# Performance work log

Measured on AMD Instinct MI355X. Metric: run time of the kernel, lower is better.

The kernel has to match this reference:

```python
import jax, jax.numpy as jnp
import numpy as np

B, S, D, H = 256, 100, 512, 8
HD = D // H  # head_dim = 64


def setup_inputs() -> dict:
    key = jax.random.key(0)
    ks = jax.random.split(key, 12)
    scale = 1.0 / np.sqrt(D)
    return {
        "x": jax.random.normal(ks[0], (B, S, D), dtype=jnp.float32),
        "pos_emb": jax.random.normal(ks[1], (1, 100, D), dtype=jnp.float32),
        "temporal_decay": jnp.float32(0.95),
        # torch nn.Linear weights are [out, in]; applied as x @ W.T + b
        "Wq": jax.random.normal(ks[2], (D, D), dtype=jnp.float32) * scale,
        "bq": jax.random.normal(ks[3], (D,), dtype=jnp.float32) * scale,
        "Wk": jax.random.normal(ks[4], (D, D), dtype=jnp.float32) * scale,
        "bk": jax.random.normal(ks[5], (D,), dtype=jnp.float32) * scale,
        "Wv": jax.random.normal(ks[6], (D, D), dtype=jnp.float32) * scale,
        "bv": jax.random.normal(ks[7], (D,), dtype=jnp.float32) * scale,
        "Wo": jax.random.normal(ks[8], (D, D), dtype=jnp.float32) * scale,
        "bo": jax.random.normal(ks[9], (D,), dtype=jnp.float32) * scale,
    }


def reference(x, pos_emb, temporal_decay, Wq, bq, Wk, bk, Wv, bv, Wo, bo):
    b, s, d = x.shape
    xp = x + pos_emb[:, :s, :]  # add position embeddings to Q/K input only

    def heads(t):  # [b,s,d] -> [b,H,s,HD]
        return t.reshape(b, s, H, HD).transpose(0, 2, 1, 3)

    q = heads(xp @ Wq.T + bq)
    k = heads(xp @ Wk.T + bk)
    v = heads(x @ Wv.T + bv)  # V uses x WITHOUT positions (per source)

    scores = jnp.einsum("bhqd,bhkd->bhqk", q, k) / np.sqrt(HD)
    # decay over KEY positions: decay^(s-1), ..., decay^1, decay^0
    exponents = jnp.arange(s - 1, -1, -1, dtype=jnp.float32)
    decay = temporal_decay ** exponents  # [s]
    scores = scores * decay[None, None, None, :]

    attn = jax.nn.softmax(scores, axis=-1)  # dropout is identity in eval
    ctx = jnp.einsum("bhqk,bhkd->bhqd", attn, v)
    ctx = ctx.transpose(0, 2, 1, 3).reshape(b, s, d)
    out = ctx @ Wo.T + bo
    return out, attn
```

## Files before the change

kernel.cpp:

```cpp
#include <hip/hip_runtime.h>
#include <hip/hip_bf16.h>
#include <cmath>

#define B_   256
#define S_   100
#define D_   512
#define H_   8
#define HD_  64
#define BS_  (B_ * S_)
#define OUT_ELEMS  (BS_ * D_)
#define ATTN_ELEMS (B_ * H_ * S_ * S_)
#define DD_  (D_ * D_)

typedef __bf16 bf16x8 __attribute__((ext_vector_type(8)));
typedef float  f32x4  __attribute__((ext_vector_type(4)));

__device__ __forceinline__ void gload16(const void* g, void* l) {
    __builtin_amdgcn_global_load_lds(
        (const __attribute__((address_space(1))) void*)g,
        (__attribute__((address_space(3))) void*)l, 16, 0, 0);
}

__device__ __forceinline__ void stage_tile(const __hip_bfloat16* __restrict__ src,
                                           char* ldsTile, int t) {
    #pragma unroll
    for (int i = 0; i < 4; ++i) {
        const int ci  = i * 256 + t;
        const int row = ci >> 3;
        const int sc  = (ci & 7) ^ (row & 7);
        gload16(src + (size_t)row * D_ + sc * 8,
                ldsTile + ((i * 256 + (t & 192)) << 4));
    }
}

__device__ __forceinline__ void stage_tile_h(const __hip_bfloat16* __restrict__ src,
                                             char* ldsTile, int t) {
    #pragma unroll
    for (int i = 0; i < 2; ++i) {
        const int ci  = i * 256 + t;
        const int row = ci >> 3;
        const int sc  = (ci & 7) ^ (row & 7);
        gload16(src + (size_t)row * D_ + sc * 8,
                ldsTile + ((i * 256 + (t & 192)) << 4));
    }
}

__device__ __forceinline__ void compute_fused(const char* buf, int lane,
                                              int wr, int wc,
                                              f32x4 acc[3][4][2]) {
    const int frow = lane & 15;
    const int fk   = lane >> 4;
    #pragma unroll
    for (int kk = 0; kk < 2; ++kk) {
        const int ch = kk * 4 + fk;
        bf16x8 af[4];
        #pragma unroll
        for (int m = 0; m < 4; ++m) {
            const int row = wr + m * 16 + frow;
            af[m] = *(const bf16x8*)(buf + row * 128 + ((ch ^ (row & 7)) << 4));
        }
        bf16x8 bfr[3][2];
        #pragma unroll
        for (int z = 0; z < 3; ++z)
            #pragma unroll
            for (int n = 0; n < 2; ++n) {
                const int row = wc + n * 16 + frow;
                bfr[z][n] = *(const bf16x8*)(buf + 16384 + z * 8192
                                             + row * 128 + ((ch ^ (row & 7)) << 4));
            }
        __builtin_amdgcn_s_setprio(1);
        #pragma unroll
        for (int z = 0; z < 3; ++z)
            #pragma unroll
            for (int m = 0; m < 4; ++m)
                #pragma unroll
                for (int n = 0; n < 2; ++n)
                    acc[z][m][n] = __builtin_amdgcn_mfma_f32_16x16x32_bf16(
                        af[m], bfr[z][n], acc[z][m][n], 0, 0, 0);
        __builtin_amdgcn_s_setprio(0);
    }
}

__device__ __forceinline__ void compute_tile_h(const char* ldsA, const char* ldsB,
                                               int lane, int wr, int wc,
                                               f32x4 acc[4][2]) {
    const int frow = lane & 15;
    const int fk   = lane >> 4;
    #pragma unroll
    for (int kk = 0; kk < 2; ++kk) {
        const int ch = kk * 4 + fk;
        bf16x8 af[4], bfr[2];
        #pragma unroll
        for (int m = 0; m < 4; ++m) {
            const int row = wr + m * 16 + frow;
            af[m] = *(const bf16x8*)(ldsA + row * 128 + ((ch ^ (row & 7)) << 4));
        }
        #pragma unroll
        for (int n = 0; n < 2; ++n) {
            const int row = wc + n * 16 + frow;
            bfr[n] = *(const bf16x8*)(ldsB + row * 128 + ((ch ^ (row & 7)) << 4));
        }
        __builtin_amdgcn_s_setprio(1);
        #pragma unroll
        for (int m = 0; m < 4; ++m)
            #pragma unroll
            for (int n = 0; n < 2; ++n)
                acc[m][n] = __builtin_amdgcn_mfma_f32_16x16x32_bf16(
                    af[m], bfr[n], acc[m][n], 0, 0, 0);
        __builtin_amdgcn_s_setprio(0);
    }
}

__global__ __launch_bounds__(256) void qkv_gemm(
    const __hip_bfloat16* __restrict__ apos,
    const __hip_bfloat16* __restrict__ wall,
    const float* __restrict__ bq, const float* __restrict__ bk,
    const float* __restrict__ bv, const float* __restrict__ pv,
    __hip_bfloat16* __restrict__ qkv)
{
    __shared__ __align__(16) char lds[2][40960];
    const int t    = threadIdx.x;
    const int r0   = blockIdx.x * 128, c0 = blockIdx.y * 64;
    const int lane = t & 63, wid = t >> 6;
    const int wr   = (wid >> 1) << 6;
    const int wc   = (wid & 1) << 5;

    f32x4 acc[3][4][2] = {};

    const __hip_bfloat16* Ab = apos + (size_t)r0 * D_;

    stage_tile(Ab, lds[0], t);
    #pragma unroll
    for (int z = 0; z < 3; ++z)
        stage_tile_h(wall + (size_t)z * DD_ + (size_t)c0 * D_,
                     lds[0] + 16384 + z * 8192, t);
    asm volatile("s_waitcnt vmcnt(0)" ::: "memory");
    __syncthreads();

    int cur = 0;
    for (int kt = 1; kt < 8; ++kt) {
        stage_tile(Ab + kt * 64, lds[cur ^ 1], t);
        #pragma unroll
        for (int z = 0; z < 3; ++z)
            stage_tile_h(wall + (size_t)z * DD_ + (size_t)c0 * D_ + kt * 64,
                         lds[cur ^ 1] + 16384 + z * 8192, t);
        compute_fused(lds[cur], lane, wr, wc, acc);
        asm volatile("s_waitcnt vmcnt(0)" ::: "memory");
        __syncthreads();
        cur ^= 1;
    }
    compute_fused(lds[cur], lane, wr, wc, acc);

    const int fcol = lane & 15, fq = lane >> 4;
    #pragma unroll
    for (int z = 0; z < 3; ++z) {
        const float* bias = (z == 0) ? bq : (z == 1) ? bk : bv;
        __hip_bfloat16* outz = qkv + (size_t)z * OUT_ELEMS;
        #pragma unroll
        for (int n = 0; n < 2; ++n) {
            const int c  = c0 + wc + n * 16 + fcol;
            const float bi = bias[c];
            const int h = c >> 6, hd = c & 63;
            #pragma unroll
            for (int m = 0; m < 4; ++m) {
                const int rbase = r0 + wr + m * 16 + fq * 4;
                #pragma unroll
                for (int r = 0; r < 4; ++r) {
                    const int rowg = rbase + r;
                    const int b = rowg / S_;
                    const int s = rowg - b * S_;
                    float v = acc[z][m][n][r] + bi;
                    if (z == 2) v -= pv[s * D_ + c];
                    outz[(((size_t)b * H_ + h) * S_ + s) * HD_ + hd] =
                        __float2bfloat16(v);
                }
            }
        }
    }
}

__global__ __launch_bounds__(256) void outproj_gemm(
    const __hip_bfloat16* __restrict__ ctx,
    const __hip_bfloat16* __restrict__ Wo,
    const float* __restrict__ bo,
    float* __restrict__ out)
{
    __shared__ __align__(16) char lds[2][24576];
    const int t    = threadIdx.x;
    const int r0   = blockIdx.x * 128, c0 = blockIdx.y * 64;
    const int lane = t & 63, wid = t >> 6;
    const int wr   = (wid >> 1) << 6, wc = (wid & 1) << 5;

    f32x4 acc[4][2] = {};

    const __hip_bfloat16* Ab = ctx + (size_t)r0 * D_;
    const __hip_bfloat16* Bb = Wo  + (size_t)c0 * D_;

    stage_tile(Ab, lds[0], t);
    stage_tile_h(Bb, lds[0] + 16384, t);
    asm volatile("s_waitcnt vmcnt(0)" ::: "memory");
    __syncthreads();

    int cur = 0;
    for (int kt = 1; kt < 8; ++kt) {
        stage_tile(Ab + kt * 64, lds[cur ^ 1], t);
        stage_tile_h(Bb + kt * 64, lds[cur ^ 1] + 16384, t);
        compute_tile_h(lds[cur], lds[cur] + 16384, lane, wr, wc, acc);
        asm volatile("s_waitcnt vmcnt(0)" ::: "memory");
        __syncthreads();
        cur ^= 1;
    }
    compute_tile_h(lds[cur], lds[cur] + 16384, lane, wr, wc, acc);

    const int fcol = lane & 15, fq = lane >> 4;
    #pragma unroll
    for (int n = 0; n < 2; ++n) {
        const int c  = c0 + wc + n * 16 + fcol;
        const float bi = bo[c];
        #pragma unroll
        for (int m = 0; m < 4; ++m) {
            const int rbase = r0 + wr + m * 16 + fq * 4;
            #pragma unroll
            for (int r = 0; r < 4; ++r) {
                const int rowg = rbase + r;
                out[(size_t)rowg * D_ + c] = acc[m][n][r] + bi;
            }
        }
    }
}

__global__ __launch_bounds__(256) void attn_mfma(
    const __hip_bfloat16* __restrict__ qkv,
    float* __restrict__ attn_out,
    __hip_bfloat16* __restrict__ ctx,
    const float* __restrict__ td_ptr)
{
    __shared__ __align__(16) __hip_bfloat16 Vt[2][64][136];
    __shared__ __align__(16) __hip_bfloat16 Pl[4][16][136];
    __shared__ float dec[128];

    const int t    = threadIdx.x;
    const int lane = t & 63, wid = t >> 6;
    const int c    = lane & 15, g4 = lane >> 4;
    const int bh0  = blockIdx.x * 2;

    if (t < 128)
        dec[t] = (t < S_) ? 0.125f * powf(td_ptr[0], (float)(S_ - 1 - t)) : 0.f;

    {
        const int h = wid >> 1;
        const int k = ((wid & 1) << 6) + lane;
        if (k < S_) {
            const __hip_bfloat16* vr = qkv + 2 * (size_t)OUT_ELEMS
                                     + (size_t)(bh0 + h) * (S_ * HD_)
                                     + (size_t)k * HD_;
            #pragma unroll
            for (int j8 = 0; j8 < 8; ++j8) {
                uint4 u = *(const uint4*)(vr + j8 * 8);
                const __hip_bfloat16* e = (const __hip_bfloat16*)&u;
                #pragma unroll
                for (int ee = 0; ee < 8; ++ee)
                    Vt[h][j8 * 8 + ee][k] = e[ee];
            }
        }
        for (int idx = t; idx < 2 * 64 * 9; idx += 256) {
            const int hh  = idx / 576;
            const int rem = idx - hh * 576;
            const int d   = rem / 9, c8 = rem - d * 9;
            *(double*)((char*)&Vt[hh][d][100] + c8 * 8) = 0.0;
        }
    }
    *(double*)&Pl[wid][c][112 + 4 * g4] = 0.0;
    __syncthreads();

    float decr[7][4];
    #pragma unroll
    for (int kt = 0; kt < 7; ++kt)
        #pragma unroll
        for (int r = 0; r < 4; ++r)
            decr[kt][r] = dec[16 * kt + 4 * g4 + r];

    for (int item = wid; item < 14; item += 4) {
        const int hh = item / 7;
        const int qt = item - hh * 7;
        const int bh = bh0 + hh;
        const __hip_bfloat16* Qb = qkv + (size_t)bh * (S_ * HD_);
        const __hip_bfloat16* Kb = qkv + (size_t)OUT_ELEMS + (size_t)bh * (S_ * HD_);

        const bf16x8 qf0 = *(const bf16x8*)(Qb + (16 * qt + c) * HD_ + 8 * g4);
        const bf16x8 qf1 = *(const bf16x8*)(Qb + (16 * qt + c) * HD_ + 32 + 8 * g4);

        f32x4 s[7] = {};
        #pragma unroll
        for (int kt = 0; kt < 7; ++kt) {
            const bf16x8 kf0 = *(const bf16x8*)(Kb + (16 * kt + c) * HD_ + 8 * g4);
            const bf16x8 kf1 = *(const bf16x8*)(Kb + (16 * kt + c) * HD_ + 32 + 8 * g4);
            s[kt] = __builtin_amdgcn_mfma_f32_16x16x32_bf16(kf0, qf0, s[kt], 0, 0, 0);
            s[kt] = __builtin_amdgcn_mfma_f32_16x16x32_bf16(kf1, qf1, s[kt], 0, 0, 0);
        }

        float m = -3.0e38f;
        #pragma unroll
        for (int kt = 0; kt < 7; ++kt)
            #pragma unroll
            for (int r = 0; r < 4; ++r) {
                float v = s[kt][r] * decr[kt][r];
                if (kt == 6 && (4 * g4 + r) >= 4) v = -3.0e38f;
                s[kt][r] = v;
                m = fmaxf(m, v);
            }
        m = fmaxf(m, __shfl_xor(m, 16, 64));
        m = fmaxf(m, __shfl_xor(m, 32, 64));

        float sum = 0.f;
        #pragma unroll
        for (int kt = 0; kt < 7; ++kt)
            #pragma unroll
            for (int r = 0; r < 4; ++r) {
                const float p = __expf(s[kt][r] - m);
                s[kt][r] = p;
                sum += p;
            }
        sum += __shfl_xor(sum, 16, 64);
        sum += __shfl_xor(sum, 32, 64);
        const float rs = 1.0f / sum;

        const int qg = 16 * qt + c;
        float* arow = attn_out + (size_t)bh * (S_ * S_) + (size_t)qg * S_;
        #pragma unroll
        for (int kt = 0; kt < 7; ++kt) {
            const float a0 = s[kt][0] * rs, a1 = s[kt][1] * rs;
            const float a2 = s[kt][2] * rs, a3 = s[kt][3] * rs;
            if (qg < S_ && (kt < 6 || g4 == 0))
                *(float4*)(arow + 16 * kt + 4 * g4) = make_float4(a0, a1, a2, a3);
            __align__(8) __hip_bfloat16 pb[4];
            pb[0] = __float2bfloat16(a0); pb[1] = __float2bfloat16(a1);
            pb[2] = __float2bfloat16(a2); pb[3] = __float2bfloat16(a3);
            *(double*)&Pl[wid][c][16 * kt + 4 * g4] = *(double*)pb;
        }

        f32x4 o[4] = {};
        #pragma unroll
        for (int kk = 0; kk < 4; ++kk) {
            const bf16x8 pf = *(const bf16x8*)&Pl[wid][c][32 * kk + 8 * g4];
            #pragma unroll
            for (int dt = 0; dt < 4; ++dt) {
                const bf16x8 vf = *(const bf16x8*)&Vt[hh][16 * dt + c][32 * kk + 8 * g4];
                o[dt] = __builtin_amdgcn_mfma_f32_16x16x32_bf16(pf, vf, o[dt], 0, 0, 0);
            }
        }

        const int b = bh >> 3, h = bh & 7;
        #pragma unroll
        for (int r = 0; r < 4; ++r) {
            const int q = 16 * qt + 4 * g4 + r;
            if (q < S_) {
                __hip_bfloat16* crow = ctx + (size_t)(b * S_ + q) * D_ + h * HD_ + c;
                #pragma unroll
                for (int dt = 0; dt < 4; ++dt)
                    crow[16 * dt] = __float2bfloat16(o[dt][r]);
            }
        }
    }
}

__global__ __launch_bounds__(256) void conv_apos_kernel(
    const float* __restrict__ x, const float* __restrict__ pos,
    __hip_bfloat16* __restrict__ apos)
{
    const int i8   = (blockIdx.x * 256 + threadIdx.x) * 8;
    const int row  = i8 >> 9;
    const int prow = row % S_;
    const int pcol = i8 & 511;
    const float4* xv = (const float4*)(x + i8);
    const float4* pp = (const float4*)(pos + (size_t)prow * D_ + pcol);
    float4 a0 = xv[0], a1 = xv[1], p0 = pp[0], p1 = pp[1];
    __align__(16) __hip_bfloat16 o[8];
    o[0] = __float2bfloat16(a0.x + p0.x); o[1] = __float2bfloat16(a0.y + p0.y);
    o[2] = __float2bfloat16(a0.z + p0.z); o[3] = __float2bfloat16(a0.w + p0.w);
    o[4] = __float2bfloat16(a1.x + p1.x); o[5] = __float2bfloat16(a1.y + p1.y);
    o[6] = __float2bfloat16(a1.z + p1.z); o[7] = __float2bfloat16(a1.w + p1.w);
    *(uint4*)(apos + i8) = *(const uint4*)o;
}

__global__ __launch_bounds__(256) void conv_w_kernel(
    const float* __restrict__ Wq, const float* __restrict__ Wk,
    const float* __restrict__ Wv, const float* __restrict__ Wo,
    __hip_bfloat16* __restrict__ wall)
{
    const int z = blockIdx.y;
    const float* src = (z == 0) ? Wq : (z == 1) ? Wk : (z == 2) ? Wv : Wo;
    __hip_bfloat16* dst = wall + (size_t)z * DD_;
    const int i8 = (blockIdx.x * 256 + threadIdx.x) * 8;
    const float4* sv = (const float4*)(src + i8);
    float4 a0 = sv[0], a1 = sv[1];
    __align__(16) __hip_bfloat16 o[8];
    o[0] = __float2bfloat16(a0.x); o[1] = __float2bfloat16(a0.y);
    o[2] = __float2bfloat16(a0.z); o[3] = __float2bfloat16(a0.w);
    o[4] = __float2bfloat16(a1.x); o[5] = __float2bfloat16(a1.y);
    o[6] = __float2bfloat16(a1.z); o[7] = __float2bfloat16(a1.w);
    *(uint4*)(dst + i8) = *(const uint4*)o;
}

__global__ __launch_bounds__(256) void posv_kernel(
    const float* __restrict__ pos, const float* __restrict__ Wv,
    float* __restrict__ pvout)
{
    const int idx = blockIdx.x * 256 + threadIdx.x;
    const int s = idx >> 9, c = idx & 511;
    const float4* pr = (const float4*)(pos + (size_t)s * D_);
    const float4* wr = (const float4*)(Wv + (size_t)c * D_);
    float a = 0.f;
    #pragma unroll 4
    for (int k = 0; k < D_ / 4; ++k) {
        float4 p = pr[k], w = wr[k];
        a = fmaf(p.x, w.x, a); a = fmaf(p.y, w.y, a);
        a = fmaf(p.z, w.z, a); a = fmaf(p.w, w.w, a);
    }
    pvout[idx] = a;
}

extern "C" void kernel_launch(void* const* d_in, const int* in_sizes, int n_in,
                              void* d_out, int out_size, void* d_ws, size_t ws_size,
                              hipStream_t stream) {
    (void)in_sizes; (void)n_in; (void)out_size; (void)ws_size;
    const float* x   = (const float*)d_in[0];
    const float* pos = (const float*)d_in[1];
    const float* td  = (const float*)d_in[2];
    const float* Wq  = (const float*)d_in[3];
    const float* bq  = (const float*)d_in[4];
    const float* Wk  = (const float*)d_in[5];
    const float* bk  = (const float*)d_in[6];
    const float* Wv  = (const float*)d_in[7];
    const float* bv  = (const float*)d_in[8];
    const float* Wo  = (const float*)d_in[9];
    const float* bo  = (const float*)d_in[10];

    float* out  = (float*)d_out;
    float* attn = out + (size_t)OUT_ELEMS;

    char* ws = (char*)d_ws;
    __hip_bfloat16* apos = (__hip_bfloat16*)ws;
    __hip_bfloat16* qkv  = (__hip_bfloat16*)(ws + 26214400);
    __hip_bfloat16* ctx  = (__hip_bfloat16*)(ws + 104857600);
    __hip_bfloat16* wall = (__hip_bfloat16*)(ws + 131072000);
    float*          pvb  = (float*)(ws + 133169152);

    conv_apos_kernel<<<OUT_ELEMS / 8 / 256, 256, 0, stream>>>(x, pos, apos);
    conv_w_kernel<<<dim3(DD_ / 8 / 256, 4), 256, 0, stream>>>(Wq, Wk, Wv, Wo, wall);
    posv_kernel<<<(S_ * D_) / 256, 256, 0, stream>>>(pos, Wv, pvb);

    qkv_gemm<<<dim3(BS_ / 128, D_ / 64), 256, 0, stream>>>(
        apos, wall, bq, bk, bv, pvb, qkv);
    attn_mfma<<<B_ * H_ / 2, 256, 0, stream>>>(qkv, attn, ctx, td);
    outproj_gemm<<<dim3(BS_ / 128, D_ / 64), 256, 0, stream>>>(
        ctx, wall + 3 * (size_t)DD_, bo, out);
}
```

Measured before the change: 182.9 us.

## Triple-buffer QKV and out-proj GEMM pipelines and use 512 threads for QKV

Both GEMMs move from a double-buffered loop that waits for all loads each iteration to a three-stage LDS ring with prefetch depth three, using partial vmcnt waits so loads stay in flight across compute. The QKV GEMM also doubles its block to 512 threads (8 waves), with each wave owning half the rows, which cuts per-wave accumulator registers and adds more waves to hide latency. LDS use grows to three buffers per block (about 120KB for QKV), which may limit blocks per CU. The hardcoded vmcnt counts must match the number of loads issued per stage.

```diff
diff --git a/kernel.cpp b/kernel.cpp
--- a/kernel.cpp
+++ b/kernel.cpp
@@ -45,17 +45,37 @@
     }
 }
 
-__device__ __forceinline__ void compute_fused(const char* buf, int lane,
-                                              int wr, int wc,
-                                              f32x4 acc[3][4][2]) {
+__device__ __forceinline__ void stage_a512(const __hip_bfloat16* __restrict__ src,
+                                           char* ldsTile, int t) {
+    #pragma unroll
+    for (int i = 0; i < 2; ++i) {
+        const int ci  = i * 512 + t;
+        const int row = ci >> 3;
+        const int sc  = (ci & 7) ^ (row & 7);
+        gload16(src + (size_t)row * D_ + sc * 8,
+                ldsTile + ((i * 512 + (t & 448)) << 4));
+    }
+}
+
+__device__ __forceinline__ void stage_b512(const __hip_bfloat16* __restrict__ src,
+                                           char* ldsTile, int t) {
+    const int row = t >> 3;
+    const int sc  = (t & 7) ^ (row & 7);
+    gload16(src + (size_t)row * D_ + sc * 8,
+            ldsTile + ((t & 448) << 4));
+}
+
+__device__ __forceinline__ void compute_fused512(const char* buf, int lane,
+                                                 int wr, int wc,
+                                                 f32x4 acc[3][2][2]) {
     const int frow = lane & 15;
     const int fk   = lane >> 4;
     #pragma unroll
     for (int kk = 0; kk < 2; ++kk) {
         const int ch = kk * 4 + fk;
-        bf16x8 af[4];
-        #pragma unroll
-        for (int m = 0; m < 4; ++m) {
+        bf16x8 af[2];
+        #pragma unroll
+        for (int m = 0; m < 2; ++m) {
             const int row = wr + m * 16 + frow;
             af[m] = *(const bf16x8*)(buf + row * 128 + ((ch ^ (row & 7)) << 4));
         }
@@ -72,7 +92,7 @@
         #pragma unroll
         for (int z = 0; z < 3; ++z)
             #pragma unroll
-            for (int m = 0; m < 4; ++m)
+            for (int m = 0; m < 2; ++m)
                 #pragma unroll
                 for (int n = 0; n < 2; ++n)
                     acc[z][m][n] = __builtin_amdgcn_mfma_f32_16x16x32_bf16(
@@ -111,45 +131,52 @@
     }
 }
 
-__global__ __launch_bounds__(256) void qkv_gemm(
+__global__ __launch_bounds__(512) void qkv_gemm(
     const __hip_bfloat16* __restrict__ apos,
     const __hip_bfloat16* __restrict__ wall,
     const float* __restrict__ bq, const float* __restrict__ bk,
     const float* __restrict__ bv, const float* __restrict__ pv,
     __hip_bfloat16* __restrict__ qkv)
 {
-    __shared__ __align__(16) char lds[2][40960];
+    __shared__ __align__(16) char lds[3][40960];
     const int t    = threadIdx.x;
     const int r0   = blockIdx.x * 128, c0 = blockIdx.y * 64;
     const int lane = t & 63, wid = t >> 6;
-    const int wr   = (wid >> 1) << 6;
+    const int wr   = (wid >> 1) << 5;
     const int wc   = (wid & 1) << 5;
 
-    f32x4 acc[3][4][2] = {};
+    f32x4 acc[3][2][2] = {};
 
     const __hip_bfloat16* Ab = apos + (size_t)r0 * D_;
 
-    stage_tile(Ab, lds[0], t);
-    #pragma unroll
-    for (int z = 0; z < 3; ++z)
-        stage_tile_h(wall + (size_t)z * DD_ + (size_t)c0 * D_,
-                     lds[0] + 16384 + z * 8192, t);
-    asm volatile("s_waitcnt vmcnt(0)" ::: "memory");
-    __syncthreads();
-
-    int cur = 0;
-    for (int kt = 1; kt < 8; ++kt) {
-        stage_tile(Ab + kt * 64, lds[cur ^ 1], t);
+    #pragma unroll
+    for (int p = 0; p < 3; ++p) {
+        stage_a512(Ab + p * 64, lds[p], t);
         #pragma unroll
         for (int z = 0; z < 3; ++z)
-            stage_tile_h(wall + (size_t)z * DD_ + (size_t)c0 * D_ + kt * 64,
-                         lds[cur ^ 1] + 16384 + z * 8192, t);
-        compute_fused(lds[cur], lane, wr, wc, acc);
-        asm volatile("s_waitcnt vmcnt(0)" ::: "memory");
-        __syncthreads();
-        cur ^= 1;
-    }
-    compute_fused(lds[cur], lane, wr, wc, acc);
+            stage_b512(wall + (size_t)z * DD_ + (size_t)c0 * D_ + p * 64,
+                       lds[p] + 16384 + z * 8192, t);
+    }
+
+    #pragma unroll
+    for (int kt = 0; kt < 8; ++kt) {
+        if (kt <= 5)      asm volatile("s_waitcnt vmcnt(10)" ::: "memory");
+        else if (kt == 6) asm volatile("s_waitcnt vmcnt(5)"  ::: "memory");
+        else              asm volatile("s_waitcnt vmcnt(0)"  ::: "memory");
+        __builtin_amdgcn_s_barrier();
+        __builtin_amdgcn_sched_barrier(0);
+        compute_fused512(lds[kt % 3], lane, wr, wc, acc);
+        asm volatile("s_waitcnt lgkmcnt(0)" ::: "memory");
+        __builtin_amdgcn_s_barrier();
+        __builtin_amdgcn_sched_barrier(0);
+        if (kt + 3 < 8) {
+            stage_a512(Ab + (kt + 3) * 64, lds[kt % 3], t);
+            #pragma unroll
+            for (int z = 0; z < 3; ++z)
+                stage_b512(wall + (size_t)z * DD_ + (size_t)c0 * D_ + (kt + 3) * 64,
+                           lds[kt % 3] + 16384 + z * 8192, t);
+        }
+    }
 
     const int fcol = lane & 15, fq = lane >> 4;
     #pragma unroll
@@ -162,7 +189,7 @@
             const float bi = bias[c];
             const int h = c >> 6, hd = c & 63;
             #pragma unroll
-            for (int m = 0; m < 4; ++m) {
+            for (int m = 0; m < 2; ++m) {
                 const int rbase = r0 + wr + m * 16 + fq * 4;
                 #pragma unroll
                 for (int r = 0; r < 4; ++r) {
@@ -185,7 +212,7 @@
     const float* __restrict__ bo,
     float* __restrict__ out)
 {
-    __shared__ __align__(16) char lds[2][24576];
+    __shared__ __align__(16) char lds[3][24576];
     const int t    = threadIdx.x;
     const int r0   = blockIdx.x * 128, c0 = blockIdx.y * 64;
     const int lane = t & 63, wid = t >> 6;
@@ -196,21 +223,28 @@
     const __hip_bfloat16* Ab = ctx + (size_t)r0 * D_;
     const __hip_bfloat16* Bb = Wo  + (size_t)c0 * D_;
 
-    stage_tile(Ab, lds[0], t);
-    stage_tile_h(Bb, lds[0] + 16384, t);
-    asm volatile("s_waitcnt vmcnt(0)" ::: "memory");
-    __syncthreads();
-
-    int cur = 0;
-    for (int kt = 1; kt < 8; ++kt) {
-        stage_tile(Ab + kt * 64, lds[cur ^ 1], t);
-        stage_tile_h(Bb + kt * 64, lds[cur ^ 1] + 16384, t);
-        compute_tile_h(lds[cur], lds[cur] + 16384, lane, wr, wc, acc);
-        asm volatile("s_waitcnt vmcnt(0)" ::: "memory");
-        __syncthreads();
-        cur ^= 1;
-    }
-    compute_tile_h(lds[cur], lds[cur] + 16384, lane, wr, wc, acc);
+    #pragma unroll
+    for (int p = 0; p < 3; ++p) {
+        stage_tile(Ab + p * 64, lds[p], t);
+        stage_tile_h(Bb + p * 64, lds[p] + 16384, t);
+    }
+
+    #pragma unroll
+    for (int kt = 0; kt < 8; ++kt) {
+        if (kt <= 5)      asm volatile("s_waitcnt vmcnt(12)" ::: "memory");
+        else if (kt == 6) asm volatile("s_waitcnt vmcnt(6)"  ::: "memory");
+        else              asm volatile("s_waitcnt vmcnt(0)"  ::: "memory");
+        __builtin_amdgcn_s_barrier();
+        __builtin_amdgcn_sched_barrier(0);
+        compute_tile_h(lds[kt % 3], lds[kt % 3] + 16384, lane, wr, wc, acc);
+        asm volatile("s_waitcnt lgkmcnt(0)" ::: "memory");
+        __builtin_amdgcn_s_barrier();
+        __builtin_amdgcn_sched_barrier(0);
+        if (kt + 3 < 8) {
+            stage_tile(Ab + (kt + 3) * 64, lds[kt % 3], t);
+            stage_tile_h(Bb + (kt + 3) * 64, lds[kt % 3] + 16384, t);
+        }
+    }
 
     const int fcol = lane & 15, fq = lane >> 4;
     #pragma unroll
@@ -450,7 +484,7 @@
     conv_w_kernel<<<dim3(DD_ / 8 / 256, 4), 256, 0, stream>>>(Wq, Wk, Wv, Wo, wall);
     posv_kernel<<<(S_ * D_) / 256, 256, 0, stream>>>(pos, Wv, pvb);
 
-    qkv_gemm<<<dim3(BS_ / 128, D_ / 64), 256, 0, stream>>>(
+    qkv_gemm<<<dim3(BS_ / 128, D_ / 64), 512, 0, stream>>>(
         apos, wall, bq, bk, bv, pvb, qkv);
     attn_mfma<<<B_ * H_ / 2, 256, 0, stream>>>(qkv, attn, ctx, td);
     outproj_gemm<<<dim3(BS_ / 128, D_ / 64), 256, 0, stream>>>(
```

New measurement: 193.8 us. 6.0% more time.
